# Performance work log

Measured on AMD Instinct MI355X. Metric: run time of the kernel, lower is better.

## Reference

```python
import jax, jax.numpy as jnp
import numpy as np

MAX_ITERS = 10


def setup_inputs() -> dict:
    key = jax.random.key(0)
    k1, k2, k3, k4, k5 = jax.random.split(key, 5)
    B, D, H = 8192, 2048, 2048
    s = 1.0 / np.sqrt(H)  # torch default init scale (uniform); we use scaled normal
    return {
        "encoded": jax.random.normal(k1, (B, D), dtype=jnp.float32),
        "w_ih": jax.random.normal(k2, (3 * H, D), dtype=jnp.float32) * s,
        "w_hh": jax.random.normal(k3, (3 * H, H), dtype=jnp.float32) * s,
        "b_ih": jax.random.normal(k4, (3 * H,), dtype=jnp.float32) * s,
        "b_hh": jax.random.normal(k5, (3 * H,), dtype=jnp.float32) * s,
    }


def reference(encoded, w_ih, w_hh, b_ih, b_hh):
    """Iterative GRUCell recurrence (training-mode: full max_iters, no early exit).

    PyTorch GRUCell math:
      r = sigmoid(W_ir x + b_ir + W_hr h + b_hr)
      z = sigmoid(W_iz x + b_iz + W_hz h + b_hz)
      n = tanh(W_in x + b_in + r * (W_hn h + b_hn))
      h' = (1 - z) * n + z * h
    """
    H = w_hh.shape[1]
    # Input projection is constant across iterations (gru_input never changes).
    gi = encoded @ w_ih.T + b_ih  # [B, 3H]
    gi_r, gi_z, gi_n = gi[:, :H], gi[:, H:2 * H], gi[:, 2 * H:]

    def step(h, _):
        gh = h @ w_hh.T + b_hh  # [B, 3H]
        gh_r, gh_z, gh_n = gh[:, :H], gh[:, H:2 * H], gh[:, 2 * H:]
        r = jax.nn.sigmoid(gi_r + gh_r)
        z = jax.nn.sigmoid(gi_z + gh_z)
        n = jnp.tanh(gi_n + r * gh_n)
        h_next = (1.0 - z) * n + z * h
        return h_next, None

    h0 = jnp.zeros((encoded.shape[0], H), dtype=encoded.dtype)
    h, _ = jax.lax.scan(step, h0, None, length=MAX_ITERS)
    return h
```

## Files before the change

kernel.cpp:

```cpp
#include <hip/hip_runtime.h>

typedef _Float16 f16_t;
typedef _Float16 f16x4 __attribute__((ext_vector_type(4)));
typedef _Float16 f16x8 __attribute__((ext_vector_type(8)));
typedef float floatx4 __attribute__((ext_vector_type(4)));

#define GLDS16(gptr, lptr) __builtin_amdgcn_global_load_lds( \
    (const __attribute__((address_space(1))) void*)(gptr),   \
    (__attribute__((address_space(3))) void*)(lptr), 16, 0, 0)

__device__ __forceinline__ float sigmoidf_fast(float x) {
    return 1.f / (1.f + __expf(-x));
}
__device__ __forceinline__ float tanhf_fast(float x) {
    float e = __expf(2.f * x);
    return 1.f - 2.f / (e + 1.f);
}

#define GATE_STRIDE 16777216L

__global__ __launch_bounds__(256)
void cvt_f32_f16(const float* __restrict__ in, f16_t* __restrict__ out, long n)
{
    long i = ((long)blockIdx.x * 256 + threadIdx.x) * 8;
    if (i >= n) return;
    floatx4 a = *(const floatx4*)(in + i);
    floatx4 b = *(const floatx4*)(in + i + 4);
    f16x8 o;
    o[0] = (f16_t)a[0]; o[1] = (f16_t)a[1]; o[2] = (f16_t)a[2]; o[3] = (f16_t)a[3];
    o[4] = (f16_t)b[0]; o[5] = (f16_t)b[1]; o[6] = (f16_t)b[2]; o[7] = (f16_t)b[3];
    *(f16x8*)(out + i) = o;
}

__device__ __forceinline__ void stage_AW(const f16_t* __restrict__ Asrc,
                                         const f16_t* __restrict__ Wsrc,
                                         f16_t* Asb, f16_t* Wsb,
                                         int m0, int n0, int kk,
                                         int wave, int srow8, int sgk)
{
    const int K = 2048, H = 2048;
    #pragma unroll
    for (int j = 0; j < 4; ++j) {
        int c = j * 4 + wave;
        int row = c * 8 + srow8;
        GLDS16(Asrc + (size_t)(m0 + row) * K + kk + sgk, Asb + c * 512);
    }
    #pragma unroll
    for (int j = 0; j < 6; ++j) {
        int c = j * 4 + wave;
        int g = c >> 3;
        int cw = c & 7;
        int row = cw * 8 + srow8;
        GLDS16(Wsrc + (size_t)(g * H + n0 + row) * K + kk + sgk,
               Wsb + c * 512);
    }
}

__global__ __launch_bounds__(256, 2)
void gemm_gi(const f16_t* __restrict__ A,
             const f16_t* __restrict__ W,
             const float* __restrict__ bias,
             f16_t* __restrict__ giF)
{
    const int H = 2048;
    __shared__ __align__(16) f16_t smem[2 * 20480];
    const int tid  = threadIdx.x;
    const int lane = tid & 63;
    const int wave = tid >> 6;

    const int bid   = blockIdx.x;
    const int xcd   = bid & 7;
    const int rblk  = bid >> 3;
    const int m0 = (rblk >> 2) * 128;
    const int n0 = (xcd * 4 + (rblk & 3)) * 64;

    const int wm = (wave >> 1) * 64;
    const int wn = (wave & 1) * 32;

    floatx4 acc[3][4][2] = {};

    const int srow8 = lane >> 3;
    const int sgk   = ((lane & 7) ^ srow8) * 8;
    const int fr = lane & 15;
    const int jq = lane >> 4;
    const int rq = (lane >> 4) * 4;

    stage_AW(A, W, smem, smem + 8192, m0, n0, 0, wave, srow8, sgk);
    __syncthreads();

    for (int t = 0; t < 32; ++t) {
        f16_t* As  = smem + (t & 1) * 20480;
        f16_t* Wsm = As + 8192;
        if (t < 31) {
            f16_t* Asn = smem + ((t + 1) & 1) * 20480;
            stage_AW(A, W, Asn, Asn + 8192, m0, n0, (t + 1) * 64,
                     wave, srow8, sgk);
        }

        #pragma unroll
        for (int ksub = 0; ksub < 2; ++ksub) {
            f16x8 a_frag[4];
            #pragma unroll
            for (int u = 0; u < 4; ++u) {
                int row = wm + u * 16 + fr;
                int slot = (ksub * 4 + jq) ^ (row & 7);
                a_frag[u] = *(const f16x8*)(As + row * 64 + slot * 8);
            }
            #pragma unroll
            for (int g = 0; g < 3; ++g) {
                #pragma unroll
                for (int tn = 0; tn < 2; ++tn) {
                    int row_w = wn + tn * 16 + fr;
                    int slot = (ksub * 4 + jq) ^ (row_w & 7);
                    f16x8 b_frag = *(const f16x8*)(Wsm + g * 4096 +
                                                   row_w * 64 + slot * 8);
                    #pragma unroll
                    for (int tm = 0; tm < 4; ++tm)
                        acc[g][tm][tn] = __builtin_amdgcn_mfma_f32_16x16x32_f16(
                            a_frag[tm], b_frag, acc[g][tm][tn], 0, 0, 0);
                }
            }
        }
        __syncthreads();
    }

    #pragma unroll
    for (int tm = 0; tm < 4; ++tm) {
        int tM = (m0 + wm + tm * 16) >> 4;
        #pragma unroll
        for (int tn = 0; tn < 2; ++tn) {
            int tN = ((n0 + wn) >> 4) + tn;
            int n  = n0 + wn + tn * 16 + fr;
            #pragma unroll
            for (int g = 0; g < 3; ++g) {
                float b = bias[g * H + n];
                f16x4 v;
                #pragma unroll
                for (int r = 0; r < 4; ++r) v[r] = (f16_t)(acc[g][tm][tn][r] + b);
                *(f16x4*)(giF + ((size_t)(g * 512 + tM) * 128 + tN) * 256 +
                          lane * 4) = v;
            }
        }
    }
}

__global__ __launch_bounds__(256)
void gru_init(const f16_t* __restrict__ giF,
              const float* __restrict__ bhh,
              f16_t* __restrict__ h16)
{
    const int H = 2048;
    __shared__ __align__(16) f16_t hp[128 * 72];
    const int tid  = threadIdx.x;
    const int lane = tid & 63;
    const int wave = tid >> 6;
    const int m0 = blockIdx.x * 128;
    const int n0 = blockIdx.y * 64;
    const int wm = (wave >> 1) * 64;
    const int wn = (wave & 1) * 32;
    const int colL = lane & 15;
    const int rq = (lane >> 4) * 4;

    #pragma unroll
    for (int tm = 0; tm < 4; ++tm) {
        int tM = (m0 + wm + tm * 16) >> 4;
        #pragma unroll
        for (int tn = 0; tn < 2; ++tn) {
            int tN = ((n0 + wn) >> 4) + tn;
            size_t base = ((size_t)tM * 128 + tN) * 256 + lane * 4;
            f16x4 g_r = *(const f16x4*)(giF + base);
            f16x4 g_z = *(const f16x4*)(giF + base + GATE_STRIDE);
            f16x4 g_n = *(const f16x4*)(giF + base + 2 * GATE_STRIDE);
            int n = n0 + wn + tn * 16 + colL;
            float br = bhh[n], bz = bhh[H + n], bn = bhh[2 * H + n];
            #pragma unroll
            for (int r = 0; r < 4; ++r) {
                float rr = sigmoidf_fast((float)g_r[r] + br);
                float zz = sigmoidf_fast((float)g_z[r] + bz);
                float nn = tanhf_fast((float)g_n[r] + rr * bn);
                float h = (1.f - zz) * nn;
                hp[(wm + tm * 16 + rq + r) * 72 + wn + tn * 16 + colL] = (f16_t)h;
            }
        }
    }
    __syncthreads();
    #pragma unroll
    for (int i = 0; i < 4; ++i) {
        int r2 = i * 32 + (tid >> 3);
        int ch = tid & 7;
        f16x8 v = *(const f16x8*)(hp + r2 * 72 + ch * 8);
        *(f16x8*)(h16 + (size_t)(m0 + r2) * H + n0 + ch * 8) = v;
    }
}

__global__ __launch_bounds__(256, 2)
void gru_step(const f16_t* __restrict__ Wh,
              const float* __restrict__ bhh,
              const f16_t* __restrict__ giF,
              const f16_t* __restrict__ hin,
              f16_t* __restrict__ hout,
              float* __restrict__ out32)
{
    const int H = 2048;
    __shared__ __align__(16) f16_t smem[2 * 20480];
    const int tid  = threadIdx.x;
    const int lane = tid & 63;
    const int wave = tid >> 6;

    const int bid   = blockIdx.x;
    const int xcd   = bid & 7;
    const int rblk  = bid >> 3;
    const int m0 = (rblk >> 2) * 128;
    const int n0 = (xcd * 4 + (rblk & 3)) * 64;

    const int wm = (wave >> 1) * 64;
    const int wn = (wave & 1) * 32;

    floatx4 acc[3][4][2] = {};

    const int srow8 = lane >> 3;
    const int sgk   = ((lane & 7) ^ srow8) * 8;
    const int fr = lane & 15;
    const int jq = lane >> 4;
    const int rq = (lane >> 4) * 4;

    f16x4 hold16[4][2];

    stage_AW(hin, Wh, smem, smem + 8192, m0, n0, 0, wave, srow8, sgk);
    __syncthreads();

    for (int t = 0; t < 32; ++t) {
        const int k0 = t * 64;
        f16_t* As  = smem + (t & 1) * 20480;
        f16_t* Wsm = As + 8192;
        if (t < 31) {
            f16_t* Asn = smem + ((t + 1) & 1) * 20480;
            stage_AW(hin, Wh, Asn, Asn + 8192, m0, n0, k0 + 64,
                     wave, srow8, sgk);
        }

        if (k0 == n0) {
            #pragma unroll
            for (int tm = 0; tm < 4; ++tm) {
                #pragma unroll
                for (int tn = 0; tn < 2; ++tn) {
                    #pragma unroll
                    for (int r = 0; r < 4; ++r) {
                        int row_a = wm + tm * 16 + rq + r;
                        int kloc  = wn + tn * 16 + fr;
                        int slot  = (kloc >> 3) ^ (row_a & 7);
                        hold16[tm][tn][r] =
                            As[row_a * 64 + slot * 8 + (kloc & 7)];
                    }
                }
            }
        }

        #pragma unroll
        for (int ksub = 0; ksub < 2; ++ksub) {
            f16x8 a_frag[4];
            #pragma unroll
            for (int u = 0; u < 4; ++u) {
                int row = wm + u * 16 + fr;
                int slot = (ksub * 4 + jq) ^ (row & 7);
                a_frag[u] = *(const f16x8*)(As + row * 64 + slot * 8);
            }
            #pragma unroll
            for (int g = 0; g < 3; ++g) {
                #pragma unroll
                for (int tn = 0; tn < 2; ++tn) {
                    int row_w = wn + tn * 16 + fr;
                    int slot = (ksub * 4 + jq) ^ (row_w & 7);
                    f16x8 b_frag = *(const f16x8*)(Wsm + g * 4096 +
                                                   row_w * 64 + slot * 8);
                    #pragma unroll
                    for (int tm = 0; tm < 4; ++tm)
                        acc[g][tm][tn] = __builtin_amdgcn_mfma_f32_16x16x32_f16(
                            a_frag[tm], b_frag, acc[g][tm][tn], 0, 0, 0);
                }
            }
        }
        __syncthreads();
    }

    f16x4 hv[4][2];
    #pragma unroll
    for (int tm = 0; tm < 4; ++tm) {
        int tM = (m0 + wm + tm * 16) >> 4;
        #pragma unroll
        for (int tn = 0; tn < 2; ++tn) {
            int tN = ((n0 + wn) >> 4) + tn;
            size_t base = ((size_t)tM * 128 + tN) * 256 + lane * 4;
            f16x4 g_r = *(const f16x4*)(giF + base);
            f16x4 g_z = *(const f16x4*)(giF + base + GATE_STRIDE);
            f16x4 g_n = *(const f16x4*)(giF + base + 2 * GATE_STRIDE);
            int n = n0 + wn + tn * 16 + fr;
            float br = bhh[n], bz = bhh[H + n], bn = bhh[2 * H + n];
            #pragma unroll
            for (int r = 0; r < 4; ++r) {
                int m = m0 + wm + tm * 16 + rq + r;
                float rr = sigmoidf_fast((float)g_r[r] + acc[0][tm][tn][r] + br);
                float zz = sigmoidf_fast((float)g_z[r] + acc[1][tm][tn][r] + bz);
                float nn = tanhf_fast((float)g_n[r] +
                                      rr * (acc[2][tm][tn][r] + bn));
                float hold = (float)hold16[tm][tn][r];
                float hnew = (1.f - zz) * nn + zz * hold;
                hv[tm][tn][r] = (f16_t)hnew;
                if (out32) out32[(size_t)m * H + n] = hnew;
            }
        }
    }

    if (!out32) {
        f16_t* hp = smem;
        #pragma unroll
        for (int tm = 0; tm < 4; ++tm)
            #pragma unroll
            for (int tn = 0; tn < 2; ++tn)
                #pragma unroll
                for (int r = 0; r < 4; ++r)
                    hp[(wm + tm * 16 + rq + r) * 72 + wn + tn * 16 + fr] =
                        hv[tm][tn][r];
        __syncthreads();
        #pragma unroll
        for (int i = 0; i < 4; ++i) {
            int r2 = i * 32 + (tid >> 3);
            int ch = tid & 7;
            f16x8 v = *(const f16x8*)(hp + r2 * 72 + ch * 8);
            *(f16x8*)(hout + (size_t)(m0 + r2) * H + n0 + ch * 8) = v;
        }
    }
}

extern "C" void kernel_launch(void* const* d_in, const int* in_sizes, int n_in,
                              void* d_out, int out_size, void* d_ws, size_t ws_size,
                              hipStream_t stream) {
    const float* x    = (const float*)d_in[0];
    const float* w_ih = (const float*)d_in[1];
    const float* w_hh = (const float*)d_in[2];
    const float* b_ih = (const float*)d_in[3];
    const float* b_hh = (const float*)d_in[4];
    float* out = (float*)d_out;

    char* ws = (char*)d_ws;
    f16_t* xh    = (f16_t*)(ws);
    f16_t* wih_h = (f16_t*)(ws + 33554432);
    f16_t* whh_h = (f16_t*)(ws + 33554432 + 25165824);
    f16_t* gi    = (f16_t*)(ws + 33554432 + 2 * 25165824);
    f16_t* h16a  = (f16_t*)(ws + 33554432 + 2 * 25165824 + 100663296);
    f16_t* h16b  = (f16_t*)(ws + 33554432 + 2 * 25165824 + 100663296 + 33554432);

    cvt_f32_f16<<<dim3(8192), 256, 0, stream>>>(x, xh, 16777216L);
    cvt_f32_f16<<<dim3(6144), 256, 0, stream>>>(w_ih, wih_h, 12582912L);
    cvt_f32_f16<<<dim3(6144), 256, 0, stream>>>(w_hh, whh_h, 12582912L);

    gemm_gi<<<dim3(2048), 256, 0, stream>>>(xh, wih_h, b_ih, gi);
    gru_init<<<dim3(64, 32), 256, 0, stream>>>(gi, b_hh, h16a);

    f16_t* hin = h16a; f16_t* hout = h16b;
    for (int it = 2; it <= 10; ++it) {
        float* o32 = (it == 10) ? out : nullptr;
        gru_step<<<dim3(2048), 256, 0, stream>>>(whh_h, b_hh, gi,
                                                 hin, hout, o32);
        f16_t* t = hin; hin = hout; hout = t;
    }
}
```

Measured before the change: 2.314 ms.

## Load A fragments straight from global into registers, stage only W in LDS

Both GEMM kernels stop staging the activation tile A in shared memory. Each wave now loads its A fragments directly from global memory into registers every k-step, while W is still double-buffered through LDS. This shrinks LDS per block so launch bounds can go from 2 to 3 blocks per CU, and gru_step reads the old hidden state directly from global. The cost is that the global A loads are issued but not prefetched ahead, so their latency sits in the MFMA loop. A tiles shared between the two waves in a row are also fetched twice, and register pressure under the tighter launch bound may cause spills.

```diff
diff --git a/kernel.cpp b/kernel.cpp
--- a/kernel.cpp
+++ b/kernel.cpp
@@ -32,19 +32,12 @@
     *(f16x8*)(out + i) = o;
 }
 
-__device__ __forceinline__ void stage_AW(const f16_t* __restrict__ Asrc,
-                                         const f16_t* __restrict__ Wsrc,
-                                         f16_t* Asb, f16_t* Wsb,
-                                         int m0, int n0, int kk,
-                                         int wave, int srow8, int sgk)
+__device__ __forceinline__ void stage_W(const f16_t* __restrict__ Wsrc,
+                                        f16_t* Wsb,
+                                        int n0, int kk,
+                                        int wave, int srow8, int sgk)
 {
     const int K = 2048, H = 2048;
-    #pragma unroll
-    for (int j = 0; j < 4; ++j) {
-        int c = j * 4 + wave;
-        int row = c * 8 + srow8;
-        GLDS16(Asrc + (size_t)(m0 + row) * K + kk + sgk, Asb + c * 512);
-    }
     #pragma unroll
     for (int j = 0; j < 6; ++j) {
         int c = j * 4 + wave;
@@ -56,14 +49,24 @@
     }
 }
 
-__global__ __launch_bounds__(256, 2)
+#define LOADA_G(dst, src, mbase, k0) do {                                    \
+    _Pragma("unroll")                                                        \
+    for (int ks_ = 0; ks_ < 2; ++ks_)                                        \
+        _Pragma("unroll")                                                    \
+        for (int tm_ = 0; tm_ < 4; ++tm_)                                    \
+            dst[ks_][tm_] = *(const f16x8*)((src) +                          \
+                (size_t)((mbase) + tm_ * 16 + fr) * 2048 +                   \
+                (k0) + ks_ * 32 + jq * 8);                                   \
+} while (0)
+
+__global__ __launch_bounds__(256, 3)
 void gemm_gi(const f16_t* __restrict__ A,
              const f16_t* __restrict__ W,
              const float* __restrict__ bias,
              f16_t* __restrict__ giF)
 {
     const int H = 2048;
-    __shared__ __align__(16) f16_t smem[2 * 20480];
+    __shared__ __align__(16) f16_t smem[2 * 12288];
     const int tid  = threadIdx.x;
     const int lane = tid & 63;
     const int wave = tid >> 6;
@@ -85,29 +88,22 @@
     const int jq = lane >> 4;
     const int rq = (lane >> 4) * 4;
 
-    stage_AW(A, W, smem, smem + 8192, m0, n0, 0, wave, srow8, sgk);
+    stage_W(W, smem, n0, 0, wave, srow8, sgk);
     __syncthreads();
 
     for (int t = 0; t < 32; ++t) {
-        f16_t* As  = smem + (t & 1) * 20480;
-        f16_t* Wsm = As + 8192;
-        if (t < 31) {
-            f16_t* Asn = smem + ((t + 1) & 1) * 20480;
-            stage_AW(A, W, Asn, Asn + 8192, m0, n0, (t + 1) * 64,
-                     wave, srow8, sgk);
-        }
-
-        #pragma unroll
-        for (int ksub = 0; ksub < 2; ++ksub) {
-            f16x8 a_frag[4];
-            #pragma unroll
-            for (int u = 0; u < 4; ++u) {
-                int row = wm + u * 16 + fr;
-                int slot = (ksub * 4 + jq) ^ (row & 7);
-                a_frag[u] = *(const f16x8*)(As + row * 64 + slot * 8);
-            }
-            #pragma unroll
-            for (int g = 0; g < 3; ++g) {
+        const int k0 = t * 64;
+        f16_t* Wsm = smem + (t & 1) * 12288;
+        f16x8 a[2][4];
+        LOADA_G(a, A, m0 + wm, k0);
+        if (t < 31)
+            stage_W(W, smem + ((t + 1) & 1) * 12288, n0, k0 + 64,
+                    wave, srow8, sgk);
+
+        #pragma unroll
+        for (int ksub = 0; ksub < 2; ++ksub)
+            #pragma unroll
+            for (int g = 0; g < 3; ++g)
                 #pragma unroll
                 for (int tn = 0; tn < 2; ++tn) {
                     int row_w = wn + tn * 16 + fr;
@@ -117,10 +113,8 @@
                     #pragma unroll
                     for (int tm = 0; tm < 4; ++tm)
                         acc[g][tm][tn] = __builtin_amdgcn_mfma_f32_16x16x32_f16(
-                            a_frag[tm], b_frag, acc[g][tm][tn], 0, 0, 0);
+                            a[ksub][tm], b_frag, acc[g][tm][tn], 0, 0, 0);
                 }
-            }
-        }
         __syncthreads();
     }
 
@@ -193,7 +187,7 @@
     }
 }
 
-__global__ __launch_bounds__(256, 2)
+__global__ __launch_bounds__(256, 3)
 void gru_step(const f16_t* __restrict__ Wh,
               const float* __restrict__ bhh,
               const f16_t* __restrict__ giF,
@@ -202,7 +196,7 @@
               float* __restrict__ out32)
 {
     const int H = 2048;
-    __shared__ __align__(16) f16_t smem[2 * 20480];
+    __shared__ __align__(16) f16_t smem[2 * 12288];
     const int tid  = threadIdx.x;
     const int lane = tid & 63;
     const int wave = tid >> 6;
@@ -225,48 +219,32 @@
     const int rq = (lane >> 4) * 4;
 
     f16x4 hold16[4][2];
-
-    stage_AW(hin, Wh, smem, smem + 8192, m0, n0, 0, wave, srow8, sgk);
+    #pragma unroll
+    for (int tm = 0; tm < 4; ++tm)
+        #pragma unroll
+        for (int tn = 0; tn < 2; ++tn)
+            #pragma unroll
+            for (int r = 0; r < 4; ++r)
+                hold16[tm][tn][r] =
+                    hin[(size_t)(m0 + wm + tm * 16 + rq + r) * H +
+                        n0 + wn + tn * 16 + fr];
+
+    stage_W(Wh, smem, n0, 0, wave, srow8, sgk);
     __syncthreads();
 
     for (int t = 0; t < 32; ++t) {
         const int k0 = t * 64;
-        f16_t* As  = smem + (t & 1) * 20480;
-        f16_t* Wsm = As + 8192;
-        if (t < 31) {
-            f16_t* Asn = smem + ((t + 1) & 1) * 20480;
-            stage_AW(hin, Wh, Asn, Asn + 8192, m0, n0, k0 + 64,
-                     wave, srow8, sgk);
-        }
-
-        if (k0 == n0) {
-            #pragma unroll
-            for (int tm = 0; tm < 4; ++tm) {
-                #pragma unroll
-                for (int tn = 0; tn < 2; ++tn) {
-                    #pragma unroll
-                    for (int r = 0; r < 4; ++r) {
-                        int row_a = wm + tm * 16 + rq + r;
-                        int kloc  = wn + tn * 16 + fr;
-                        int slot  = (kloc >> 3) ^ (row_a & 7);
-                        hold16[tm][tn][r] =
-                            As[row_a * 64 + slot * 8 + (kloc & 7)];
-                    }
-                }
-            }
-        }
-
-        #pragma unroll
-        for (int ksub = 0; ksub < 2; ++ksub) {
-            f16x8 a_frag[4];
-            #pragma unroll
-            for (int u = 0; u < 4; ++u) {
-                int row = wm + u * 16 + fr;
-                int slot = (ksub * 4 + jq) ^ (row & 7);
-                a_frag[u] = *(const f16x8*)(As + row * 64 + slot * 8);
-            }
-            #pragma unroll
-            for (int g = 0; g < 3; ++g) {
+        f16_t* Wsm = smem + (t & 1) * 12288;
+        f16x8 a[2][4];
+        LOADA_G(a, hin, m0 + wm, k0);
+        if (t < 31)
+            stage_W(Wh, smem + ((t + 1) & 1) * 12288, n0, k0 + 64,
+                    wave, srow8, sgk);
+
+        #pragma unroll
+        for (int ksub = 0; ksub < 2; ++ksub)
+            #pragma unroll
+            for (int g = 0; g < 3; ++g)
                 #pragma unroll
                 for (int tn = 0; tn < 2; ++tn) {
                     int row_w = wn + tn * 16 + fr;
@@ -276,10 +254,8 @@
                     #pragma unroll
                     for (int tm = 0; tm < 4; ++tm)
                         acc[g][tm][tn] = __builtin_amdgcn_mfma_f32_16x16x32_f16(
-                            a_frag[tm], b_frag, acc[g][tm][tn], 0, 0, 0);
+                            a[ksub][tm], b_frag, acc[g][tm][tn], 0, 0, 0);
                 }
-            }
-        }
         __syncthreads();
     }
 
```

Measured after the change: 3.650 ms. +57.7%, slower.
